# Optimization experiments

Hardware: AMD Instinct MI355X
Metric: run time of the kernel (lower is better)

Reference implementation:

```python
import jax, jax.numpy as jnp
import numpy as np

B = 64        # graphs per batch
NPG = 1024    # nodes per graph
N = B * NPG
K = 8         # knn neighbors
H = 128       # Config.hidden_dim
FDIM = 32     # input_dim - 1
OUT = 2
NEG_SLOPE = 0.2


def setup_inputs() -> dict:
    key = jax.random.key(0)
    ks = jax.random.split(key, 24)
    rn = lambda k, shp, s=0.05: jax.random.normal(k, shp, jnp.float32) * s
    inp = {
        "x": jax.random.normal(ks[0], (N, FDIM + 1), jnp.float32),
        "batch": (jnp.arange(N, dtype=jnp.int32) // NPG),
        # initial_mlp: Linear(FDIM, H)
        "w0": rn(ks[1], (FDIM, H)), "b0": rn(ks[2], (H,)),
        # conv1: mlp Linear(2H+1,H)->ReLU->Linear(H,H); gate Linear(2H+1,H)->Sigmoid
        "c1_mw1": rn(ks[3], (2 * H + 1, H)), "c1_mb1": rn(ks[4], (H,)),
        "c1_mw2": rn(ks[5], (H, H)),         "c1_mb2": rn(ks[6], (H,)),
        "c1_gw": rn(ks[7], (2 * H + 1, H)),  "c1_gb": rn(ks[8], (H,)),
        # conv2
        "c2_mw1": rn(ks[9], (2 * H + 1, H)), "c2_mb1": rn(ks[10], (H,)),
        "c2_mw2": rn(ks[11], (H, H)),        "c2_mb2": rn(ks[12], (H,)),
        "c2_gw": rn(ks[13], (2 * H + 1, H)), "c2_gb": rn(ks[14], (H,)),
        # classifier: Linear(2H,H)->ReLU->Linear(H,OUT)
        "cw1": rn(ks[15], (2 * H, H)), "cb1": rn(ks[16], (H,)),
        "cw2": rn(ks[17], (H, OUT)),   "cb2": rn(ks[18], (OUT,)),
    }
    return inp


def _knn_graph(xh):
    """Per-graph kNN (loop=False). xh: [N, H]. Returns global neighbor idx [N, K]."""
    xg = xh.reshape(B, NPG, -1)
    sq = jnp.sum(xg * xg, axis=-1)                              # [B, NPG]
    d2 = sq[:, :, None] + sq[:, None, :] - 2.0 * jnp.einsum('bnh,bmh->bnm', xg, xg)
    d2 = d2 + jnp.eye(NPG, dtype=xh.dtype) * 1e9                # exclude self-loops
    _, idx = jax.lax.top_k(-d2, K)                              # [B, NPG, K] local ids
    offs = (jnp.arange(B, dtype=idx.dtype) * NPG)[:, None, None]
    return (idx + offs).reshape(N, K)


def _highway_edge_conv(x, nbr, feat, mw1, mb1, mw2, mb2, gw, gb):
    """Gather -> edge MLP + sigmoid gate -> mean aggregation + identity skip."""
    xj = x[nbr]                                                 # [N, K, H]
    xi = jnp.broadcast_to(x[:, None, :], xj.shape)              # [N, K, H]
    fd = feat[:, None, :] - feat[nbr]                           # [N, K, 1]
    c = jnp.concatenate([xi, xj, fd], axis=-1)                  # [N, K, 2H+1]
    h = jax.nn.relu(c @ mw1 + mb1) @ mw2 + mb2
    g = jax.nn.sigmoid(c @ gw + gb)
    msg = g * h + (1.0 - g) * xj
    return msg.mean(axis=1) + x                                 # mean aggr + identity skip


def reference(x, batch, w0, b0,
              c1_mw1, c1_mb1, c1_mw2, c1_mb2, c1_gw, c1_gb,
              c2_mw1, c2_mb1, c2_mw2, c2_mb2, c2_gw, c2_gb,
              cw1, cb1, cw2, cb2):
    feat = x[:, :FDIM]                 # key_feature_idx == last column
    kf = x[:, FDIM:FDIM + 1]           # [N, 1]
    xh = jax.nn.relu(feat @ w0 + b0)   # initial_mlp (dropout inactive at eval)
    nbr = _knn_graph(xh)               # dynamic knn on embedded features
    x1 = jax.nn.leaky_relu(_highway_edge_conv(xh, nbr, kf, c1_mw1, c1_mb1, c1_mw2, c1_mb2, c1_gw, c1_gb), NEG_SLOPE)
    x2 = jax.nn.leaky_relu(_highway_edge_conv(x1, nbr, kf, c2_mw1, c2_mb1, c2_mw2, c2_mb2, c2_gw, c2_gb), NEG_SLOPE)
    xc = jnp.concatenate([x1, x2], axis=-1).reshape(B, NPG, 2 * H).max(axis=1)  # global max pool
    logits = jax.nn.relu(xc @ cw1 + cb1) @ cw2 + cb2
    return jax.nn.log_softmax(logits, axis=-1)
```

## Files before the change

### kernel.cpp

```cpp
#include <hip/hip_runtime.h>
#include <math.h>
#include <stdint.h>

#define NTOT   65536
#define NPG    1024
#define KNN    8
#define HDIM   128
#define XSTR   33
#define NEG    0.2f

typedef _Float16 h2 __attribute__((ext_vector_type(2)));
typedef short bf16x8 __attribute__((ext_vector_type(8)));
typedef float f32x4 __attribute__((ext_vector_type(4)));
typedef unsigned short u16;
typedef unsigned int u32;

#if defined(__has_builtin)
#if __has_builtin(__builtin_amdgcn_fdot2)
#define HAVE_FDOT2 1
#endif
#endif

__device__ __forceinline__ float fdot2f(h2 a, h2 b, float c) {
#ifdef HAVE_FDOT2
  return __builtin_amdgcn_fdot2(a, b, c, false);
#else
  return c + (float)a.x * (float)b.x + (float)a.y * (float)b.y;
#endif
}

__device__ __forceinline__ u16 f2bf(float f) {
  const u32 u = __builtin_bit_cast(u32, f);
  return (u16)((u + 0x7FFFu + ((u >> 16) & 1u)) >> 16);
}
__device__ __forceinline__ float bf2f(u16 h) {
  return __builtin_bit_cast(float, ((u32)h) << 16);
}
__device__ __forceinline__ void bf8_to_f(const u16* __restrict__ p, float* f) {
  const uint4 v = *reinterpret_cast<const uint4*>(p);
  const u32 w[4] = {v.x, v.y, v.z, v.w};
#pragma unroll
  for (int i = 0; i < 4; ++i) {
    f[2 * i]     = bf2f((u16)(w[i] & 0xffffu));
    f[2 * i + 1] = bf2f((u16)(w[i] >> 16));
  }
}

__global__ __launch_bounds__(256) void k_embed(const float* __restrict__ x,
                                               const float* __restrict__ w0,
                                               const float* __restrict__ b0,
                                               u16* __restrict__ xh_hi,
                                               u16* __restrict__ xh_lo,
                                               float* __restrict__ sq) {
  __shared__ float w0s[32 * HDIM];
  __shared__ float fs[2][32];
  __shared__ float red[256];
  const int tid = threadIdx.x;
  for (int i = tid; i < 32 * HDIM; i += 256) w0s[i] = w0[i];
  const int h = tid & 127;
  const int nl = tid >> 7;
  const float bias = b0[h];
  for (int it = 0; it < 16; ++it) {
    const int n = blockIdx.x * 32 + it * 2 + nl;
    __syncthreads();
    if (tid < 64) {
      const int r = tid >> 5, f = tid & 31;
      fs[r][f] = x[(size_t)(blockIdx.x * 32 + it * 2 + r) * XSTR + f];
    }
    __syncthreads();
    float acc = bias;
#pragma unroll
    for (int f = 0; f < 32; ++f) acc = fmaf(fs[nl][f], w0s[f * HDIM + h], acc);
    acc = fmaxf(acc, 0.f);
    const u16 hh = f2bf(acc);
    xh_hi[(size_t)n * HDIM + h] = hh;
    xh_lo[(size_t)n * HDIM + h] = f2bf(acc - bf2f(hh));
    red[tid] = acc * acc;
    __syncthreads();
    for (int s = 64; s > 0; s >>= 1) {
      if ((tid & 127) < s) red[tid] += red[tid + s];
      __syncthreads();
    }
    if ((tid & 127) == 0) sq[n] = red[tid];
  }
}

__global__ __launch_bounds__(256) void k_prep(const float* __restrict__ m1,
                                              const float* __restrict__ g1,
                                              const float* __restrict__ m2,
                                              const float* __restrict__ g2,
                                              u16* __restrict__ Wt) {
  const int b = blockIdx.x;
  const int layer = b >> 2, which = b & 3;
  const float* src = (layer == 0) ? ((which < 2) ? m1 : g1)
                                  : ((which < 2) ? m2 : g2);
  src += (size_t)(which & 1) * 128 * HDIM;
  u16* dst = Wt + (size_t)b * 128 * 128;
  const int t = threadIdx.x;
  const int n = t >> 1, k0 = (t & 1) * 64;
  for (int kk = 0; kk < 64; kk += 2) {
    const float f0 = src[(size_t)(k0 + kk) * HDIM + n];
    const float f1 = src[(size_t)(k0 + kk + 1) * HDIM + n];
    const u32 pk = (u32)f2bf(f0) | ((u32)f2bf(f1) << 16);
    *reinterpret_cast<u32*>(&dst[(size_t)n * 128 + k0 + kk]) = pk;
  }
}

__global__ __launch_bounds__(256) void k_knn(const u16* __restrict__ xh_hi,
                                             const u16* __restrict__ xh_lo,
                                             const float* __restrict__ sq,
                                             int* __restrict__ nbr) {
  __shared__ __align__(16) u16 BsH[32 * 128];
  __shared__ __align__(16) u16 BsL[32 * 128];
  __shared__ __align__(16) float Ds[128 * 33];
  __shared__ float sqs[32];
  const int tid = threadIdx.x;
  const int wave = tid >> 6, lane = tid & 63;
  const int fr = lane & 15, fg = lane >> 4;
  const int g = blockIdx.x >> 3;
  const int n0 = (blockIdx.x & 7) * 128;
  const int gbase = g * NPG;

  bf16x8 aH[2][4], aL[2][4];
#pragma unroll
  for (int mt = 0; mt < 2; ++mt)
#pragma unroll
    for (int kt = 0; kt < 4; ++kt) {
      const size_t off =
          (size_t)(gbase + n0 + wave * 32 + mt * 16 + fr) * HDIM + kt * 32 + fg * 8;
      aH[mt][kt] = *reinterpret_cast<const bf16x8*>(&xh_hi[off]);
      aL[mt][kt] = *reinterpret_cast<const bf16x8*>(&xh_lo[off]);
    }

  const int srow = tid >> 1, shalf = tid & 1;
  const int nglob = gbase + n0 + srow;
  float bd[8];
  int bi[8];
#pragma unroll
  for (int i = 0; i < 8; ++i) { bd[i] = 1e30f; bi[i] = 0; }

  char* BsHc = reinterpret_cast<char*>(BsH);
  char* BsLc = reinterpret_cast<char*>(BsL);

  for (int ct = 0; ct < 32; ++ct) {
    const int m0 = gbase + ct * 32;
    __syncthreads();
    if (tid < 32) sqs[tid] = sq[m0 + tid];
    {
      const int col = tid >> 3, kc = (tid & 7) * 16;
      const size_t off = (size_t)(m0 + col) * HDIM + kc;
      const uint4 h0 = *reinterpret_cast<const uint4*>(&xh_hi[off]);
      const uint4 h1 = *reinterpret_cast<const uint4*>(&xh_hi[off + 8]);
      const uint4 l0 = *reinterpret_cast<const uint4*>(&xh_lo[off]);
      const uint4 l1 = *reinterpret_cast<const uint4*>(&xh_lo[off + 8]);
      const int base = col * 256, sw = (col & 7) << 4;
      const int kb = kc * 2;
      *reinterpret_cast<uint4*>(BsHc + base + ((kb) ^ sw)) = h0;
      *reinterpret_cast<uint4*>(BsHc + base + ((kb + 16) ^ sw)) = h1;
      *reinterpret_cast<uint4*>(BsLc + base + ((kb) ^ sw)) = l0;
      *reinterpret_cast<uint4*>(BsLc + base + ((kb + 16) ^ sw)) = l1;
    }
    __syncthreads();
    f32x4 acc[2][2];
#pragma unroll
    for (int mt = 0; mt < 2; ++mt)
#pragma unroll
      for (int nt = 0; nt < 2; ++nt) acc[mt][nt] = (f32x4){0.f, 0.f, 0.f, 0.f};
#pragma unroll
    for (int nt = 0; nt < 2; ++nt) {
      bf16x8 bH[4], bL[4];
      const int col = nt * 16 + fr;
      const int base = col * 256, sw = (col & 7) << 4;
#pragma unroll
      for (int kt = 0; kt < 4; ++kt) {
        const int kb = (kt * 32 + fg * 8) * 2;
        bH[kt] = *reinterpret_cast<const bf16x8*>(BsHc + base + (kb ^ sw));
        bL[kt] = *reinterpret_cast<const bf16x8*>(BsLc + base + (kb ^ sw));
      }
#pragma unroll
      for (int mt = 0; mt < 2; ++mt)
#pragma unroll
        for (int kt = 0; kt < 4; ++kt) {
          acc[mt][nt] = __builtin_amdgcn_mfma_f32_16x16x32_bf16(
              aH[mt][kt], bH[kt], acc[mt][nt], 0, 0, 0);
          acc[mt][nt] = __builtin_amdgcn_mfma_f32_16x16x32_bf16(
              aH[mt][kt], bL[kt], acc[mt][nt], 0, 0, 0);
          acc[mt][nt] = __builtin_amdgcn_mfma_f32_16x16x32_bf16(
              aL[mt][kt], bH[kt], acc[mt][nt], 0, 0, 0);
        }
    }
#pragma unroll
    for (int mt = 0; mt < 2; ++mt)
#pragma unroll
      for (int nt = 0; nt < 2; ++nt)
#pragma unroll
        for (int r = 0; r < 4; ++r)
          Ds[(wave * 32 + mt * 16 + fg * 4 + r) * 33 + nt * 16 + fr] =
              acc[mt][nt][r];
    __syncthreads();
#pragma unroll
    for (int c2 = 0; c2 < 16; ++c2) {
      const int c = shalf * 16 + c2;
      const int m = m0 + c;
      const float d = sqs[c] - 2.f * Ds[srow * 33 + c];
      if ((m != nglob) && (d < bd[7])) {
        bd[7] = d; bi[7] = m;
#pragma unroll
        for (int q = 7; q > 0; --q) {
          if (bd[q] < bd[q - 1]) {
            const float td = bd[q]; bd[q] = bd[q - 1]; bd[q - 1] = td;
            const int ti = bi[q]; bi[q] = bi[q - 1]; bi[q - 1] = ti;
          }
        }
      }
    }
  }
  __syncthreads();
  float* mdist = Ds;
  int* midx = reinterpret_cast<int*>(BsH);
#pragma unroll
  for (int i = 0; i < 8; ++i) { mdist[tid * 8 + i] = bd[i]; midx[tid * 8 + i] = bi[i]; }
  __syncthreads();
  if (shalf == 0) {
    const float* dA = &mdist[(srow * 2) * 8];
    const float* dB = &mdist[(srow * 2 + 1) * 8];
    const int* iA = &midx[(srow * 2) * 8];
    const int* iB = &midx[(srow * 2 + 1) * 8];
    int pa = 0, pb = 0;
    int* outp = &nbr[(size_t)nglob * KNN];
#pragma unroll
    for (int i = 0; i < 8; ++i) {
      const float da = dA[pa], db = dB[pb];
      const bool takeA = (da < db) || ((da == db) && (iA[pa] < iB[pb]));
      outp[i] = takeA ? iA[pa] : iB[pb];
      if (takeA) ++pa; else ++pb;
    }
  }
}

__global__ __launch_bounds__(256) void k_ng(const u16* __restrict__ xin_b,
                                            const u16* __restrict__ WtL,
                                            const float* __restrict__ mb1,
                                            const float* __restrict__ gb,
                                            u16* __restrict__ a1,
                                            u16* __restrict__ a2,
                                            u16* __restrict__ uu,
                                            u16* __restrict__ vv) {
  const int tid = threadIdx.x;
  const int wave = tid >> 6, lane = tid & 63;
  const int fr = lane & 15, fg = lane >> 4;
  const int n0 = blockIdx.x * 128;
  const int cb = blockIdx.y;
  const u16* W = WtL + (size_t)cb * 128 * 128;
  const float* bias = (cb == 0) ? mb1 : (cb == 2) ? gb : nullptr;
  u16* outp = (cb == 0) ? a1 : (cb == 1) ? a2 : (cb == 2) ? uu : vv;

  bf16x8 afr[2][4];
#pragma unroll
  for (int mt = 0; mt < 2; ++mt)
#pragma unroll
    for (int kt = 0; kt < 4; ++kt)
      afr[mt][kt] = *reinterpret_cast<const bf16x8*>(
          &xin_b[(size_t)(n0 + wave * 32 + mt * 16 + fr) * HDIM + kt * 32 + fg * 8]);

#pragma unroll
  for (int nt = 0; nt < 8; ++nt) {
    const int col = nt * 16 + fr;
    bf16x8 bfr[4];
#pragma unroll
    for (int kt = 0; kt < 4; ++kt)
      bfr[kt] = *reinterpret_cast<const bf16x8*>(&W[(size_t)col * 128 + kt * 32 + fg * 8]);
    const float bv = bias ? bias[col] : 0.f;
#pragma unroll
    for (int mt = 0; mt < 2; ++mt) {
      f32x4 acc = (f32x4){0.f, 0.f, 0.f, 0.f};
#pragma unroll
      for (int kt = 0; kt < 4; ++kt)
        acc = __builtin_amdgcn_mfma_f32_16x16x32_bf16(afr[mt][kt], bfr[kt], acc, 0, 0, 0);
      const int rbase = n0 + wave * 32 + mt * 16 + fg * 4;
#pragma unroll
      for (int r = 0; r < 4; ++r)
        outp[(size_t)(rbase + r) * HDIM + col] = f2bf(acc[r] + bv);
    }
  }
}

__global__ __launch_bounds__(256) void k_conv(const u16* __restrict__ xin,
                                              const int* __restrict__ nbr,
                                              const float* __restrict__ xraw,
                                              const u16* __restrict__ a1,
                                              const u16* __restrict__ a2,
                                              const u16* __restrict__ uu,
                                              const u16* __restrict__ vv,
                                              const float* __restrict__ mw1,
                                              const float* __restrict__ mw2,
                                              const float* __restrict__ mb2,
                                              const float* __restrict__ gw,
                                              u16* __restrict__ xout) {
  __shared__ __align__(16) h2 Et[64][128];
  __shared__ __align__(16) h2 Ws[64][128];
  __shared__ int jn[128];
  __shared__ float fdv[128];
  __shared__ float w1rs[HDIM];
  __shared__ float gwrs[HDIM];
  const int tid = threadIdx.x;
  const int i0 = blockIdx.x * 16;

  if (tid < 128) {
    w1rs[tid] = mw1[256 * HDIM + tid];
    gwrs[tid] = gw[256 * HDIM + tid];
    const int i = i0 + (tid >> 3);
    const int j = nbr[(size_t)i * KNN + (tid & 7)];
    jn[tid] = j;
    fdv[tid] = xraw[(size_t)i * XSTR + 32] - xraw[(size_t)j * XSTR + 32];
  }
#pragma unroll
  for (int c = 0; c < 8; ++c) {
    const int s = tid + c * 256;
    const int k2 = s >> 5, h4 = s & 31;
    const float4 va = *reinterpret_cast<const float4*>(&mw2[(size_t)(2 * k2) * HDIM + h4 * 4]);
    const float4 vb = *reinterpret_cast<const float4*>(&mw2[(size_t)(2 * k2 + 1) * HDIM + h4 * 4]);
    h2 t0; t0.x = (_Float16)va.x; t0.y = (_Float16)vb.x; Ws[k2][h4 * 4 + 0] = t0;
    h2 t1; t1.x = (_Float16)va.y; t1.y = (_Float16)vb.y; Ws[k2][h4 * 4 + 1] = t1;
    h2 t2; t2.x = (_Float16)va.z; t2.y = (_Float16)vb.z; Ws[k2][h4 * 4 + 2] = t2;
    h2 t3; t3.x = (_Float16)va.w; t3.y = (_Float16)vb.w; Ws[k2][h4 * 4 + 3] = t3;
  }
  __syncthreads();
  {
    const int e = tid >> 1;
    const int kk0 = (tid & 1) * 64;
    const int inode = i0 + (e >> 3);
    const int j = jn[e];
    const float fd = fdv[e];
#pragma unroll
    for (int s8 = 0; s8 < 8; ++s8) {
      const int kk = kk0 + s8 * 8;
      float fa[8], fb[8];
      bf8_to_f(&a1[(size_t)inode * HDIM + kk], fa);
      bf8_to_f(&a2[(size_t)j * HDIM + kk], fb);
      float p[8];
#pragma unroll
      for (int q = 0; q < 8; ++q)
        p[q] = fmaxf(fa[q] + fb[q] + fd * w1rs[kk + q], 0.f);
      h2 e0; e0.x = (_Float16)p[0]; e0.y = (_Float16)p[1];
      h2 e1; e1.x = (_Float16)p[2]; e1.y = (_Float16)p[3];
      h2 e2; e2.x = (_Float16)p[4]; e2.y = (_Float16)p[5];
      h2 e3; e3.x = (_Float16)p[6]; e3.y = (_Float16)p[7];
      Et[(kk >> 1) + 0][e] = e0;
      Et[(kk >> 1) + 1][e] = e1;
      Et[(kk >> 1) + 2][e] = e2;
      Et[(kk >> 1) + 3][e] = e3;
    }
  }
  __syncthreads();
  const int ty = tid >> 4, tx = tid & 15;
  float acc[8][8];
#pragma unroll
  for (int r = 0; r < 8; ++r)
#pragma unroll
    for (int c = 0; c < 8; ++c) acc[r][c] = 0.f;
  for (int k2 = 0; k2 < 64; ++k2) {
    const uint4 uA0 = *reinterpret_cast<const uint4*>(&Et[k2][ty * 8]);
    const uint4 uA1 = *reinterpret_cast<const uint4*>(&Et[k2][ty * 8 + 4]);
    const uint4 uB0 = *reinterpret_cast<const uint4*>(&Ws[k2][tx * 8]);
    const uint4 uB1 = *reinterpret_cast<const uint4*>(&Ws[k2][tx * 8 + 4]);
    const h2 a[8] = {__builtin_bit_cast(h2, uA0.x), __builtin_bit_cast(h2, uA0.y),
                     __builtin_bit_cast(h2, uA0.z), __builtin_bit_cast(h2, uA0.w),
                     __builtin_bit_cast(h2, uA1.x), __builtin_bit_cast(h2, uA1.y),
                     __builtin_bit_cast(h2, uA1.z), __builtin_bit_cast(h2, uA1.w)};
    const h2 b[8] = {__builtin_bit_cast(h2, uB0.x), __builtin_bit_cast(h2, uB0.y),
                     __builtin_bit_cast(h2, uB0.z), __builtin_bit_cast(h2, uB0.w),
                     __builtin_bit_cast(h2, uB1.x), __builtin_bit_cast(h2, uB1.y),
                     __builtin_bit_cast(h2, uB1.z), __builtin_bit_cast(h2, uB1.w)};
#pragma unroll
    for (int r = 0; r < 8; ++r)
#pragma unroll
      for (int c = 0; c < 8; ++c) acc[r][c] = fdot2f(a[r], b[c], acc[r][c]);
  }
  const int node = i0 + ty;
  float xi_[8], ui_[8], mb2v[8], gwv[8];
  {
    bf8_to_f(&xin[(size_t)node * HDIM + tx * 8], xi_);
    bf8_to_f(&uu[(size_t)node * HDIM + tx * 8], ui_);
    const float4 m0 = *reinterpret_cast<const float4*>(&mb2[tx * 8]);
    const float4 m1 = *reinterpret_cast<const float4*>(&mb2[tx * 8 + 4]);
    mb2v[0] = m0.x; mb2v[1] = m0.y; mb2v[2] = m0.z; mb2v[3] = m0.w;
    mb2v[4] = m1.x; mb2v[5] = m1.y; mb2v[6] = m1.z; mb2v[7] = m1.w;
#pragma unroll
    for (int c = 0; c < 8; ++c) gwv[c] = gwrs[tx * 8 + c];
  }
  float msum[8];
#pragma unroll
  for (int c = 0; c < 8; ++c) msum[c] = 0.f;
#pragma unroll
  for (int r = 0; r < 8; ++r) {
    const int e = ty * 8 + r;
    const int j = jn[e];
    const float fd = fdv[e];
    float vj[8], xj[8];
    bf8_to_f(&vv[(size_t)j * HDIM + tx * 8], vj);
    bf8_to_f(&xin[(size_t)j * HDIM + tx * 8], xj);
#pragma unroll
    for (int c = 0; c < 8; ++c) {
      const float z = ui_[c] + vj[c] + fd * gwv[c];
      const float gsig = 1.f / (1.f + __expf(-z));
      const float M = acc[r][c] + mb2v[c];
      msum[c] += gsig * M + (1.f - gsig) * xj[c];
    }
  }
  u32 w[4];
#pragma unroll
  for (int i = 0; i < 4; ++i) {
    float t0 = msum[2 * i] * 0.125f + xi_[2 * i];
    float t1 = msum[2 * i + 1] * 0.125f + xi_[2 * i + 1];
    t0 = (t0 > 0.f) ? t0 : NEG * t0;
    t1 = (t1 > 0.f) ? t1 : NEG * t1;
    w[i] = (u32)f2bf(t0) | ((u32)f2bf(t1) << 16);
  }
  *reinterpret_cast<uint4*>(&xout[(size_t)node * HDIM + tx * 8]) =
      make_uint4(w[0], w[1], w[2], w[3]);
}

__global__ __launch_bounds__(256) void k_head(const u16* __restrict__ x1,
                                              const u16* __restrict__ x2,
                                              const float* __restrict__ cw1,
                                              const float* __restrict__ cb1,
                                              const float* __restrict__ cw2,
                                              const float* __restrict__ cb2,
                                              float* __restrict__ out) {
  __shared__ float xc[256];
  __shared__ float hid[128];
  __shared__ float red[128];
  const int b = blockIdx.x, t = threadIdx.x;
  const u16* src = (t < 128) ? x1 : x2;
  const int f = t & 127;
  const size_t base = (size_t)b * NPG;
  float m = -1e30f;
  for (int p = 0; p < NPG; p += 4) {
    const float v0 = bf2f(src[(base + p + 0) * HDIM + f]);
    const float v1 = bf2f(src[(base + p + 1) * HDIM + f]);
    const float v2 = bf2f(src[(base + p + 2) * HDIM + f]);
    const float v3 = bf2f(src[(base + p + 3) * HDIM + f]);
    m = fmaxf(m, fmaxf(fmaxf(v0, v1), fmaxf(v2, v3)));
  }
  xc[t] = m;
  __syncthreads();
  if (t < 128) {
    float acc = cb1[t];
    for (int f2 = 0; f2 < 256; ++f2) acc = fmaf(xc[f2], cw1[f2 * HDIM + t], acc);
    hid[t] = fmaxf(acc, 0.f);
  }
  __syncthreads();
  if (t < 128) red[t] = hid[t] * cw2[t * 2 + 0];
  __syncthreads();
  for (int s = 64; s > 0; s >>= 1) {
    if (t < s) red[t] += red[t + s];
    __syncthreads();
  }
  float l0 = 0.f;
  if (t == 0) l0 = red[0] + cb2[0];
  __syncthreads();
  if (t < 128) red[t] = hid[t] * cw2[t * 2 + 1];
  __syncthreads();
  for (int s = 64; s > 0; s >>= 1) {
    if (t < s) red[t] += red[t + s];
    __syncthreads();
  }
  if (t == 0) {
    const float l1 = red[0] + cb2[1];
    const float mm = fmaxf(l0, l1);
    const float lse = mm + logf(__expf(l0 - mm) + __expf(l1 - mm));
    out[b * 2 + 0] = l0 - lse;
    out[b * 2 + 1] = l1 - lse;
  }
}

extern "C" void kernel_launch(void* const* d_in, const int* in_sizes, int n_in,
                              void* d_out, int out_size, void* d_ws, size_t ws_size,
                              hipStream_t stream) {
  (void)in_sizes; (void)n_in; (void)out_size; (void)ws_size;
  const float* x      = (const float*)d_in[0];
  const float* w0     = (const float*)d_in[2];
  const float* b0     = (const float*)d_in[3];
  const float* c1_mw1 = (const float*)d_in[4];
  const float* c1_mb1 = (const float*)d_in[5];
  const float* c1_mw2 = (const float*)d_in[6];
  const float* c1_mb2 = (const float*)d_in[7];
  const float* c1_gw  = (const float*)d_in[8];
  const float* c1_gb  = (const float*)d_in[9];
  const float* c2_mw1 = (const float*)d_in[10];
  const float* c2_mb1 = (const float*)d_in[11];
  const float* c2_mw2 = (const float*)d_in[12];
  const float* c2_mb2 = (const float*)d_in[13];
  const float* c2_gw  = (const float*)d_in[14];
  const float* c2_gb  = (const float*)d_in[15];
  const float* cw1    = (const float*)d_in[16];
  const float* cb1    = (const float*)d_in[17];
  const float* cw2    = (const float*)d_in[18];
  const float* cb2    = (const float*)d_in[19];

  const size_t NF = (size_t)NTOT * HDIM;
  u16* wsh   = (u16*)d_ws;
  u16* xh_hi = wsh + 0 * NF;
  u16* xh_lo = wsh + 1 * NF;
  u16* x1b   = wsh + 2 * NF;
  u16* x2b   = wsh + 3 * NF;
  u16* a1v   = wsh + 4 * NF;
  u16* a2v   = wsh + 5 * NF;
  u16* uv    = wsh + 6 * NF;
  u16* vv_   = wsh + 7 * NF;
  u16* Wt    = wsh + 8 * NF;
  float* sqv = (float*)(Wt + 8 * 128 * 128);
  int* nbrv  = (int*)(sqv + NTOT);

  k_prep<<<8, 256, 0, stream>>>(c1_mw1, c1_gw, c2_mw1, c2_gw, Wt);
  k_embed<<<2048, 256, 0, stream>>>(x, w0, b0, xh_hi, xh_lo, sqv);
  k_knn<<<512, 256, 0, stream>>>(xh_hi, xh_lo, sqv, nbrv);

  k_ng<<<dim3(512, 4), 256, 0, stream>>>(xh_hi, Wt, c1_mb1, c1_gb,
                                         a1v, a2v, uv, vv_);
  k_conv<<<4096, 256, 0, stream>>>(xh_hi, nbrv, x, a1v, a2v, uv, vv_,
                                   c1_mw1, c1_mw2, c1_mb2, c1_gw, x1b);

  k_ng<<<dim3(512, 4), 256, 0, stream>>>(x1b, Wt + 4 * 128 * 128, c2_mb1, c2_gb,
                                         a1v, a2v, uv, vv_);
  k_conv<<<4096, 256, 0, stream>>>(x1b, nbrv, x, a1v, a2v, uv, vv_,
                                   c2_mw1, c2_mw2, c2_mb2, c2_gw, x2b);

  k_head<<<64, 256, 0, stream>>>(x1b, x2b, cw1, cb1, cw2, cb2, (float*)d_out);
}
```

Baseline: 796.0 us.

## Use f16 MFMA for edge second-layer GEMM in conv with pre-transposed weights

Replaces the scalar fdot2 register-tiled GEMM in k_conv with 16x16x32 f16 MFMA instructions. Edge hidden activations are built directly into register fragments, and mw2 is pre-transposed to f16 once in k_prep, so each block no longer has to convert and stage the weights in shared memory. Results go through a padded fp32 shared buffer so the existing gate/aggregation epilogue can be reused. Shared memory use grows slightly, and the weight B-fragments are now read from global/L2 by every block.

```diff
diff --git a/kernel.cpp b/kernel.cpp
--- a/kernel.cpp
+++ b/kernel.cpp
@@ -10,24 +10,11 @@
 #define NEG    0.2f
 
 typedef _Float16 h2 __attribute__((ext_vector_type(2)));
+typedef _Float16 h8 __attribute__((ext_vector_type(8)));
 typedef short bf16x8 __attribute__((ext_vector_type(8)));
 typedef float f32x4 __attribute__((ext_vector_type(4)));
 typedef unsigned short u16;
 typedef unsigned int u32;
-
-#if defined(__has_builtin)
-#if __has_builtin(__builtin_amdgcn_fdot2)
-#define HAVE_FDOT2 1
-#endif
-#endif
-
-__device__ __forceinline__ float fdot2f(h2 a, h2 b, float c) {
-#ifdef HAVE_FDOT2
-  return __builtin_amdgcn_fdot2(a, b, c, false);
-#else
-  return c + (float)a.x * (float)b.x + (float)a.y * (float)b.y;
-#endif
-}
 
 __device__ __forceinline__ u16 f2bf(float f) {
   const u32 u = __builtin_bit_cast(u32, f);
@@ -89,20 +76,34 @@
                                               const float* __restrict__ g1,
                                               const float* __restrict__ m2,
                                               const float* __restrict__ g2,
+                                              const float* __restrict__ w2a,
+                                              const float* __restrict__ w2b,
                                               u16* __restrict__ Wt) {
   const int b = blockIdx.x;
-  const int layer = b >> 2, which = b & 3;
-  const float* src = (layer == 0) ? ((which < 2) ? m1 : g1)
-                                  : ((which < 2) ? m2 : g2);
-  src += (size_t)(which & 1) * 128 * HDIM;
-  u16* dst = Wt + (size_t)b * 128 * 128;
   const int t = threadIdx.x;
   const int n = t >> 1, k0 = (t & 1) * 64;
-  for (int kk = 0; kk < 64; kk += 2) {
-    const float f0 = src[(size_t)(k0 + kk) * HDIM + n];
-    const float f1 = src[(size_t)(k0 + kk + 1) * HDIM + n];
-    const u32 pk = (u32)f2bf(f0) | ((u32)f2bf(f1) << 16);
-    *reinterpret_cast<u32*>(&dst[(size_t)n * 128 + k0 + kk]) = pk;
+  u16* dst = Wt + (size_t)b * 128 * 128;
+  if (b < 8) {
+    const int layer = b >> 2, which = b & 3;
+    const float* src = (layer == 0) ? ((which < 2) ? m1 : g1)
+                                    : ((which < 2) ? m2 : g2);
+    src += (size_t)(which & 1) * 128 * HDIM;
+    for (int kk = 0; kk < 64; kk += 2) {
+      const float f0 = src[(size_t)(k0 + kk) * HDIM + n];
+      const float f1 = src[(size_t)(k0 + kk + 1) * HDIM + n];
+      const u32 pk = (u32)f2bf(f0) | ((u32)f2bf(f1) << 16);
+      *reinterpret_cast<u32*>(&dst[(size_t)n * 128 + k0 + kk]) = pk;
+    }
+  } else {
+    const float* src = (b == 8) ? w2a : w2b;
+    for (int kk = 0; kk < 64; kk += 2) {
+      const float f0 = src[(size_t)(k0 + kk) * HDIM + n];
+      const float f1 = src[(size_t)(k0 + kk + 1) * HDIM + n];
+      const u16 h0 = __builtin_bit_cast(u16, (_Float16)f0);
+      const u16 h1 = __builtin_bit_cast(u16, (_Float16)f1);
+      const u32 pk = (u32)h0 | ((u32)h1 << 16);
+      *reinterpret_cast<u32*>(&dst[(size_t)n * 128 + k0 + kk]) = pk;
+    }
   }
 }
 
@@ -293,12 +294,11 @@
                                               const u16* __restrict__ uu,
                                               const u16* __restrict__ vv,
                                               const float* __restrict__ mw1,
-                                              const float* __restrict__ mw2,
+                                              const u16* __restrict__ mw2t,
                                               const float* __restrict__ mb2,
                                               const float* __restrict__ gw,
                                               u16* __restrict__ xout) {
-  __shared__ __align__(16) h2 Et[64][128];
-  __shared__ __align__(16) h2 Ws[64][128];
+  __shared__ __align__(16) float Ms[128 * 132];
   __shared__ int jn[128];
   __shared__ float fdv[128];
   __shared__ float w1rs[HDIM];
@@ -314,69 +314,61 @@
     jn[tid] = j;
     fdv[tid] = xraw[(size_t)i * XSTR + 32] - xraw[(size_t)j * XSTR + 32];
   }
-#pragma unroll
-  for (int c = 0; c < 8; ++c) {
-    const int s = tid + c * 256;
-    const int k2 = s >> 5, h4 = s & 31;
-    const float4 va = *reinterpret_cast<const float4*>(&mw2[(size_t)(2 * k2) * HDIM + h4 * 4]);
-    const float4 vb = *reinterpret_cast<const float4*>(&mw2[(size_t)(2 * k2 + 1) * HDIM + h4 * 4]);
-    h2 t0; t0.x = (_Float16)va.x; t0.y = (_Float16)vb.x; Ws[k2][h4 * 4 + 0] = t0;
-    h2 t1; t1.x = (_Float16)va.y; t1.y = (_Float16)vb.y; Ws[k2][h4 * 4 + 1] = t1;
-    h2 t2; t2.x = (_Float16)va.z; t2.y = (_Float16)vb.z; Ws[k2][h4 * 4 + 2] = t2;
-    h2 t3; t3.x = (_Float16)va.w; t3.y = (_Float16)vb.w; Ws[k2][h4 * 4 + 3] = t3;
-  }
-  __syncthreads();
-  {
-    const int e = tid >> 1;
-    const int kk0 = (tid & 1) * 64;
+  __syncthreads();
+
+  const int wave = tid >> 6, lane = tid & 63;
+  const int fr = lane & 15, fg = lane >> 4;
+
+  h8 efrag[2][4];
+#pragma unroll
+  for (int mt = 0; mt < 2; ++mt) {
+    const int e = wave * 32 + mt * 16 + fr;
     const int inode = i0 + (e >> 3);
     const int j = jn[e];
     const float fd = fdv[e];
 #pragma unroll
-    for (int s8 = 0; s8 < 8; ++s8) {
-      const int kk = kk0 + s8 * 8;
+    for (int kt = 0; kt < 4; ++kt) {
+      const int k0 = kt * 32 + fg * 8;
       float fa[8], fb[8];
-      bf8_to_f(&a1[(size_t)inode * HDIM + kk], fa);
-      bf8_to_f(&a2[(size_t)j * HDIM + kk], fb);
-      float p[8];
+      bf8_to_f(&a1[(size_t)inode * HDIM + k0], fa);
+      bf8_to_f(&a2[(size_t)j * HDIM + k0], fb);
+      h8 ef;
 #pragma unroll
       for (int q = 0; q < 8; ++q)
-        p[q] = fmaxf(fa[q] + fb[q] + fd * w1rs[kk + q], 0.f);
-      h2 e0; e0.x = (_Float16)p[0]; e0.y = (_Float16)p[1];
-      h2 e1; e1.x = (_Float16)p[2]; e1.y = (_Float16)p[3];
-      h2 e2; e2.x = (_Float16)p[4]; e2.y = (_Float16)p[5];
-      h2 e3; e3.x = (_Float16)p[6]; e3.y = (_Float16)p[7];
-      Et[(kk >> 1) + 0][e] = e0;
-      Et[(kk >> 1) + 1][e] = e1;
-      Et[(kk >> 1) + 2][e] = e2;
-      Et[(kk >> 1) + 3][e] = e3;
-    }
-  }
-  __syncthreads();
+        ef[q] = (_Float16)fmaxf(fa[q] + fb[q] + fd * w1rs[k0 + q], 0.f);
+      efrag[mt][kt] = ef;
+    }
+  }
+
+  f32x4 acc[2][8];
+#pragma unroll
+  for (int mt = 0; mt < 2; ++mt)
+#pragma unroll
+    for (int nt = 0; nt < 8; ++nt) acc[mt][nt] = (f32x4){0.f, 0.f, 0.f, 0.f};
+#pragma unroll
+  for (int nt = 0; nt < 8; ++nt) {
+    const int col = nt * 16 + fr;
+    h8 bfr[4];
+#pragma unroll
+    for (int kt = 0; kt < 4; ++kt)
+      bfr[kt] = *reinterpret_cast<const h8*>(&mw2t[(size_t)col * 128 + kt * 32 + fg * 8]);
+#pragma unroll
+    for (int mt = 0; mt < 2; ++mt)
+#pragma unroll
+      for (int kt = 0; kt < 4; ++kt)
+        acc[mt][nt] = __builtin_amdgcn_mfma_f32_16x16x32_f16(
+            efrag[mt][kt], bfr[kt], acc[mt][nt], 0, 0, 0);
+  }
+#pragma unroll
+  for (int mt = 0; mt < 2; ++mt)
+#pragma unroll
+    for (int nt = 0; nt < 8; ++nt)
+#pragma unroll
+      for (int r = 0; r < 4; ++r)
+        Ms[(wave * 32 + mt * 16 + fg * 4 + r) * 132 + nt * 16 + fr] = acc[mt][nt][r];
+  __syncthreads();
+
   const int ty = tid >> 4, tx = tid & 15;
-  float acc[8][8];
-#pragma unroll
-  for (int r = 0; r < 8; ++r)
-#pragma unroll
-    for (int c = 0; c < 8; ++c) acc[r][c] = 0.f;
-  for (int k2 = 0; k2 < 64; ++k2) {
-    const uint4 uA0 = *reinterpret_cast<const uint4*>(&Et[k2][ty * 8]);
-    const uint4 uA1 = *reinterpret_cast<const uint4*>(&Et[k2][ty * 8 + 4]);
-    const uint4 uB0 = *reinterpret_cast<const uint4*>(&Ws[k2][tx * 8]);
-    const uint4 uB1 = *reinterpret_cast<const uint4*>(&Ws[k2][tx * 8 + 4]);
-    const h2 a[8] = {__builtin_bit_cast(h2, uA0.x), __builtin_bit_cast(h2, uA0.y),
-                     __builtin_bit_cast(h2, uA0.z), __builtin_bit_cast(h2, uA0.w),
-                     __builtin_bit_cast(h2, uA1.x), __builtin_bit_cast(h2, uA1.y),
-                     __builtin_bit_cast(h2, uA1.z), __builtin_bit_cast(h2, uA1.w)};
-    const h2 b[8] = {__builtin_bit_cast(h2, uB0.x), __builtin_bit_cast(h2, uB0.y),
-                     __builtin_bit_cast(h2, uB0.z), __builtin_bit_cast(h2, uB0.w),
-                     __builtin_bit_cast(h2, uB1.x), __builtin_bit_cast(h2, uB1.y),
-                     __builtin_bit_cast(h2, uB1.z), __builtin_bit_cast(h2, uB1.w)};
-#pragma unroll
-    for (int r = 0; r < 8; ++r)
-#pragma unroll
-      for (int c = 0; c < 8; ++c) acc[r][c] = fdot2f(a[r], b[c], acc[r][c]);
-  }
   const int node = i0 + ty;
   float xi_[8], ui_[8], mb2v[8], gwv[8];
   {
@@ -400,11 +392,14 @@
     float vj[8], xj[8];
     bf8_to_f(&vv[(size_t)j * HDIM + tx * 8], vj);
     bf8_to_f(&xin[(size_t)j * HDIM + tx * 8], xj);
+    const float4 M0 = *reinterpret_cast<const float4*>(&Ms[e * 132 + tx * 8]);
+    const float4 M1 = *reinterpret_cast<const float4*>(&Ms[e * 132 + tx * 8 + 4]);
+    const float Mv[8] = {M0.x, M0.y, M0.z, M0.w, M1.x, M1.y, M1.z, M1.w};
 #pragma unroll
     for (int c = 0; c < 8; ++c) {
       const float z = ui_[c] + vj[c] + fd * gwv[c];
       const float gsig = 1.f / (1.f + __expf(-z));
-      const float M = acc[r][c] + mb2v[c];
+      const float M = Mv[c] + mb2v[c];
       msum[c] += gsig * M + (1.f - gsig) * xj[c];
     }
   }
@@ -510,22 +505,22 @@
   u16* uv    = wsh + 6 * NF;
   u16* vv_   = wsh + 7 * NF;
   u16* Wt    = wsh + 8 * NF;
-  float* sqv = (float*)(Wt + 8 * 128 * 128);
+  float* sqv = (float*)(Wt + 10 * 128 * 128);
   int* nbrv  = (int*)(sqv + NTOT);
 
-  k_prep<<<8, 256, 0, stream>>>(c1_mw1, c1_gw, c2_mw1, c2_gw, Wt);
+  k_prep<<<10, 256, 0, stream>>>(c1_mw1, c1_gw, c2_mw1, c2_gw, c1_mw2, c2_mw2, Wt);
   k_embed<<<2048, 256, 0, stream>>>(x, w0, b0, xh_hi, xh_lo, sqv);
   k_knn<<<512, 256, 0, stream>>>(xh_hi, xh_lo, sqv, nbrv);
 
   k_ng<<<dim3(512, 4), 256, 0, stream>>>(xh_hi, Wt, c1_mb1, c1_gb,
                                          a1v, a2v, uv, vv_);
   k_conv<<<4096, 256, 0, stream>>>(xh_hi, nbrv, x, a1v, a2v, uv, vv_,
-                                   c1_mw1, c1_mw2, c1_mb2, c1_gw, x1b);
+                                   c1_mw1, Wt + 8 * 128 * 128, c1_mb2, c1_gw, x1b);
 
   k_ng<<<dim3(512, 4), 256, 0, stream>>>(x1b, Wt + 4 * 128 * 128, c2_mb1, c2_gb,
                                          a1v, a2v, uv, vv_);
   k_conv<<<4096, 256, 0, stream>>>(x1b, nbrv, x, a1v, a2v, uv, vv_,
-                                   c2_mw1, c2_mw2, c2_mb2, c2_gw, x2b);
+                                   c2_mw1, Wt + 9 * 128 * 128, c2_mb2, c2_gw, x2b);
 
   k_head<<<64, 256, 0, stream>>>(x1b, x2b, cw1, cb1, cw2, cb2, (float*)d_out);
 }
```

New measurement: 724.8 us. 1.1x faster.
